# Performance work log

Hardware: AMD Instinct MI355X
Metric: run time of the kernel (lower is better)

The kernel has to match this reference:

```python
import jax, jax.numpy as jnp
import numpy as np

D = 512          # token_dim * num_heads
TOKEN_DIM = 256
SCALE = TOKEN_DIM ** (-0.5)


def _l2norm(x, axis):
    # torch.nn.functional.normalize: x / max(||x||_2, eps)
    n = jnp.linalg.norm(x, axis=axis, keepdims=True)
    return x / jnp.maximum(n, 1e-12)


def setup_inputs() -> dict:
    key = jax.random.key(0)
    ks = jax.random.split(key, 32)
    B, N, IN = 8, 4096, 512
    s_in = 1.0 / np.sqrt(IN)
    s_d = 1.0 / np.sqrt(D)

    def lin(k, fin, fout, scale):
        kw, kb = jax.random.split(k)
        return (jax.random.uniform(kw, (fin, fout), jnp.float32, -scale, scale),
                jax.random.uniform(kb, (fout,), jnp.float32, -scale, scale))

    wq_I, bq_I = lin(ks[0], IN, D, s_in)
    wk_I, bk_I = lin(ks[1], IN, D, s_in)
    wq_M, bq_M = lin(ks[2], IN, D, s_in)
    wk_M, bk_M = lin(ks[3], IN, D, s_in)
    p1_w, p1_b = lin(ks[4], D, D, s_d)
    p2_w, p2_b = lin(ks[5], D, D, s_d)
    p3_w, p3_b = lin(ks[6], D, D, s_d)
    p4_w, p4_b = lin(ks[7], D, D, s_d)
    f_w, f_b = lin(ks[8], D, TOKEN_DIM, s_d)
    return {
        'x_I': jax.random.normal(ks[9], (B, N, IN), jnp.float32),
        'x_M': jax.random.normal(ks[10], (B, N, IN), jnp.float32),
        'wq_I': wq_I, 'bq_I': bq_I, 'wk_I': wk_I, 'bk_I': bk_I,
        'wq_M': wq_M, 'bq_M': bq_M, 'wk_M': wk_M, 'bk_M': bk_M,
        'wg_I': jax.random.normal(ks[11], (D, 1), jnp.float32),
        'wg_M': jax.random.normal(ks[12], (D, 1), jnp.float32),
        'p1_w': p1_w, 'p1_b': p1_b, 'p2_w': p2_w, 'p2_b': p2_b,
        'p3_w': p3_w, 'p3_b': p3_b, 'p4_w': p4_w, 'p4_b': p4_b,
        'f_w': f_w, 'f_b': f_b,
    }


def reference(x_I, x_M, wq_I, bq_I, wk_I, bk_I, wq_M, bq_M, wk_M, bk_M,
              wg_I, wg_M, p1_w, p1_b, p2_w, p2_b, p3_w, p3_b, p4_w, p4_b,
              f_w, f_b):
    # projections, then L2-normalize along feature dim
    q_I = _l2norm(x_I @ wq_I + bq_I, axis=-1)   # [B, N, D]
    k_I = _l2norm(x_I @ wk_I + bk_I, axis=-1)
    q_M = _l2norm(x_M @ wq_M + bq_M, axis=-1)
    k_M = _l2norm(x_M @ wk_M + bk_M, axis=-1)

    # softmax-free attention weights, L2-normalized over sequence dim
    A_I = _l2norm((q_I @ wg_I) * SCALE, axis=1)  # [B, N, 1]
    A_M = _l2norm((q_M @ wg_M) * SCALE, axis=1)

    # pooled global queries, broadcast back over tokens
    G_I = jnp.sum(A_I * q_I, axis=1, keepdims=True)  # [B, 1, D]
    G_M = jnp.sum(A_M * q_M, axis=1, keepdims=True)

    out = ((G_I * k_I) @ p1_w + p1_b
           + (G_I * k_M) @ p2_w + p2_b
           + (G_M * k_M) @ p3_w + p3_b
           + (G_M * k_I) @ p4_w + p4_b
           + q_I + q_M)                              # [B, N, D]
    return out @ f_w + f_b                           # [B, N, token_dim]
```

## Files before the change

kernel.cpp:

```cpp
#include <hip/hip_runtime.h>

typedef unsigned short u16;
typedef unsigned int   u32;
typedef __bf16 bf16_t;
typedef bf16_t bf16x8 __attribute__((ext_vector_type(8)));
typedef float  f32x4  __attribute__((ext_vector_type(4)));

__device__ __forceinline__ float b2f(u16 u){
  u32 x = ((u32)u) << 16;
  return __builtin_bit_cast(float, x);
}
__device__ __forceinline__ u16 f2b(float f){
  u32 u = __builtin_bit_cast(u32, f);
  u32 r = u + 0x7FFFu + ((u >> 16) & 1u);
  return (u16)(r >> 16);
}

union V8 { uint4 q; u16 u[8]; };

__device__ __forceinline__ void gld16(const u16* gsrc, u16* ldst){
  __builtin_amdgcn_global_load_lds(
      (const __attribute__((address_space(1))) u32*)gsrc,
      (__attribute__((address_space(3))) u32*)ldst, 16, 0, 0);
}


struct CArgs { const float* src[4]; u16* dst[4]; int cnt[4]; };

__global__ __launch_bounds__(256) void convert_k(CArgs c){
  int z = blockIdx.z;
  int i8 = (blockIdx.x * 256 + threadIdx.x) * 8;
  if (i8 >= c.cnt[z]) return;
  const float* s = c.src[z] + i8;
  float4 a = *(const float4*)s;
  float4 b = *(const float4*)(s + 4);
  V8 o;
  o.u[0]=f2b(a.x); o.u[1]=f2b(a.y); o.u[2]=f2b(a.z); o.u[3]=f2b(a.w);
  o.u[4]=f2b(b.x); o.u[5]=f2b(b.y); o.u[6]=f2b(b.z); o.u[7]=f2b(b.w);
  *(uint4*)(c.dst[z] + i8) = o.q;
}

struct TArgs { const float* src[5]; u16* dst[5]; int ncol[5]; };

__global__ __launch_bounds__(256) void transpose_k(TArgs t,
    const float* __restrict__ p1b, const float* __restrict__ p2b,
    const float* __restrict__ p3b, const float* __restrict__ p4b,
    const float* __restrict__ fw, const float* __restrict__ fb,
    float* __restrict__ cb, float* __restrict__ Gun)
{
  __shared__ u16 T[64][65];
  __shared__ float sb[512];
  int z = blockIdx.z;
  int tid = threadIdx.x;
  if (z == 5){
    if (blockIdx.x == 0 && blockIdx.y == 0){
      sb[tid]       = p1b[tid] + p2b[tid] + p3b[tid] + p4b[tid];
      sb[tid + 256] = p1b[tid+256] + p2b[tid+256] + p3b[tid+256] + p4b[tid+256];
      __syncthreads();
      float acc = 0.f;
      for (int j = 0; j < 512; j++) acc += sb[j] * fw[j*256 + tid];
      cb[tid] = acc + fb[tid];
    } else if (blockIdx.x >= 1 && blockIdx.x <= 4){
      int idx = ((blockIdx.x - 1)*8 + blockIdx.y)*256 + tid;
      Gun[idx] = 0.f;
    }
    return;
  }
  int nc = t.ncol[z];
  int j0 = blockIdx.y * 64;
  if (j0 >= nc) return;
  int i0 = blockIdx.x * 64;
  const float* s = t.src[z];
  u16* d = t.dst[z];
  #pragma unroll
  for (int rep = 0; rep < 16; rep++){
    int lin = rep*256 + tid;
    int r = lin >> 6, c = lin & 63;
    T[c][r] = f2b(s[(size_t)(i0 + r) * nc + j0 + c]);
  }
  __syncthreads();
  #pragma unroll
  for (int rep = 0; rep < 16; rep++){
    int lin = rep*256 + tid;
    int r = lin >> 6, c = lin & 63;
    d[(size_t)(j0 + r) * 512 + i0 + c] = T[r][c];
  }
}

__global__ __launch_bounds__(256, 2) void proj_k(
    const float* __restrict__ XI, const float* __restrict__ XM,
    const u16* __restrict__ WTI, const u16* __restrict__ WTM,
    const float* __restrict__ bqI, const float* __restrict__ bkI,
    const float* __restrict__ bqM, const float* __restrict__ bkM,
    const float* __restrict__ wgI, const float* __restrict__ wgM,
    u16* __restrict__ qI, u16* __restrict__ kI,
    u16* __restrict__ qM, u16* __restrict__ kM,
    float* __restrict__ Araw, float* __restrict__ Gun)
{
  const int tid = threadIdx.x, l = tid & 63, w = tid >> 6;
  const int m0 = blockIdx.x * 64;
  const int y  = blockIdx.y, zi = blockIdx.z;
  __shared__ __align__(16) u16 As[2][64*32];
  __shared__ __align__(16) u16 Bs[2][4][4096];
  const int lr = l & 15, quad = l >> 4;
  const int srow = l >> 2;
  const int swz8 = ((l & 3) ^ ((l >> 3) & 3)) * 8;
  const int aqs8 = (quad ^ ((lr >> 1) & 3)) * 8;
  const int wn = w * 128;

  const float* X  = zi ? XM : XI;
  const u16* Wbase = (zi ? WTM : WTI) + (size_t)y * 512 * 512 + (size_t)wn * 512;
  const float* bias = y ? (zi ? bkM : bkI) : (zi ? bqM : bqI);
  const float* wg   = zi ? wgM : wgI;
  u16* OUT = y ? (zi ? kM : kI) : (zi ? qM : qI);

  const int arow = w*16 + (l >> 2);
  const int aks  = (l & 3) * 8;
  const float* aptr = X + (size_t)(m0 + arow)*512 + aks;

  f32x4 acc[4][8] = {};
  float4 s0a, s0b, s1a, s1b;

  s0a = *(const float4*)(aptr);
  s0b = *(const float4*)(aptr + 4);
  __builtin_amdgcn_sched_barrier(0);
  #pragma unroll
  for (int i = 0; i < 8; i++)
    gld16(Wbase + (size_t)(i*16 + srow)*512 + swz8, &Bs[0][w][i*512]);
  __builtin_amdgcn_sched_barrier(0);
  s1a = *(const float4*)(aptr + 32);
  s1b = *(const float4*)(aptr + 36);
  __builtin_amdgcn_sched_barrier(0);
  {
    V8 o;
    o.u[0]=f2b(s0a.x); o.u[1]=f2b(s0a.y); o.u[2]=f2b(s0a.z); o.u[3]=f2b(s0a.w);
    o.u[4]=f2b(s0b.x); o.u[5]=f2b(s0b.y); o.u[6]=f2b(s0b.z); o.u[7]=f2b(s0b.w);
    *(uint4*)&As[0][arow*32 + swz8] = o.q;
  }
  asm volatile("s_waitcnt vmcnt(2)" ::: "memory");
  asm volatile("s_waitcnt lgkmcnt(0)" ::: "memory");
  __builtin_amdgcn_sched_barrier(0);
  __builtin_amdgcn_s_barrier();

#define PBODY(P, CV0, CV1, LD0, LD1, KA, KB, DOLOAD, VMC) do{                              \
    bf16x8 aF[4], bF[8];                                                                   \
    _Pragma("unroll")                                                                      \
    for (int mt = 0; mt < 4; mt++)                                                         \
      aF[mt] = *(const bf16x8*)&As[(P)][(mt*16 + lr)*32 + aqs8];                           \
    _Pragma("unroll")                                                                      \
    for (int nt = 0; nt < 8; nt++)                                                         \
      bF[nt] = *(const bf16x8*)&Bs[(P)][w][(nt*16 + lr)*32 + aqs8];                        \
    __builtin_amdgcn_sched_barrier(0);                                                     \
    _Pragma("unroll")                                                                      \
    for (int i = 0; i < 8; i++)                                                            \
      gld16(Wbase + (size_t)(i*16 + srow)*512 + (KB) + swz8, &Bs[(P)^1][w][i*512]);        \
    __builtin_amdgcn_sched_barrier(0);                                                     \
    if (DOLOAD){                                                                           \
      LD0 = *(const float4*)(aptr + (KA));                                                 \
      LD1 = *(const float4*)(aptr + (KA) + 4);                                             \
    }                                                                                      \
    __builtin_amdgcn_sched_barrier(0);                                                     \
    { V8 o;                                                                                \
      o.u[0]=f2b((CV0).x); o.u[1]=f2b((CV0).y); o.u[2]=f2b((CV0).z); o.u[3]=f2b((CV0).w); \
      o.u[4]=f2b((CV1).x); o.u[5]=f2b((CV1).y); o.u[6]=f2b((CV1).z); o.u[7]=f2b((CV1).w); \
      *(uint4*)&As[(P)^1][arow*32 + swz8] = o.q; }                                         \
    __builtin_amdgcn_s_setprio(1);                                                         \
    _Pragma("unroll")                                                                      \
    for (int mt = 0; mt < 4; mt++){                                                        \
      _Pragma("unroll")                                                                    \
      for (int nt = 0; nt < 8; nt++)                                                       \
        acc[mt][nt] = __builtin_amdgcn_mfma_f32_16x16x32_bf16(aF[mt], bF[nt], acc[mt][nt], 0, 0, 0); \
    }                                                                                      \
    __builtin_amdgcn_s_setprio(0);                                                         \
    asm volatile("s_waitcnt vmcnt(" #VMC ")" ::: "memory");                                \
    asm volatile("s_waitcnt lgkmcnt(0)" ::: "memory");                                     \
    __builtin_amdgcn_sched_barrier(0);                                                     \
    __builtin_amdgcn_s_barrier();                                                          \
  } while(0)

  for (int tt = 0; tt < 7; ++tt){
    PBODY(0, s1a, s1b, s0a, s0b, (2*tt+2)*32, (2*tt+1)*32, 1, 2);
    PBODY(1, s0a, s0b, s1a, s1b, (2*tt+3)*32, (2*tt+2)*32, 1, 2);
  }
  PBODY(0, s1a, s1b, s0a, s0b, 0, 480, 0, 0);
  {
    bf16x8 aF[4], bF[8];
    #pragma unroll
    for (int mt = 0; mt < 4; mt++)
      aF[mt] = *(const bf16x8*)&As[1][(mt*16 + lr)*32 + aqs8];
    #pragma unroll
    for (int nt = 0; nt < 8; nt++)
      bF[nt] = *(const bf16x8*)&Bs[1][w][(nt*16 + lr)*32 + aqs8];
    __builtin_amdgcn_s_setprio(1);
    #pragma unroll
    for (int mt = 0; mt < 4; mt++){
      #pragma unroll
      for (int nt = 0; nt < 8; nt++)
        acc[mt][nt] = __builtin_amdgcn_mfma_f32_16x16x32_bf16(aF[mt], bF[nt], acc[mt][nt], 0, 0, 0);
    }
    __builtin_amdgcn_s_setprio(0);
  }
#undef PBODY

  float wgv[8];
  if (y == 0){
    #pragma unroll
    for (int nt = 0; nt < 8; nt++) wgv[nt] = wg[wn + nt*16 + lr];
  }
  #pragma unroll
  for (int nt = 0; nt < 8; nt++){
    float bcol = bias[wn + nt*16 + lr];
    #pragma unroll
    for (int mt = 0; mt < 4; mt++)
      #pragma unroll
      for (int r = 0; r < 4; r++)
        acc[mt][nt][r] += bcol;
  }
  float ss[4][4], dq[4][4];
  #pragma unroll
  for (int mt = 0; mt < 4; mt++)
    #pragma unroll
    for (int r = 0; r < 4; r++){
      float s = 0.f, d = 0.f;
      #pragma unroll
      for (int nt = 0; nt < 8; nt++){
        float v = acc[mt][nt][r];
        s += v*v;
        if (y == 0) d += v * wgv[nt];
      }
      ss[mt][r] = s; dq[mt][r] = d;
    }
  #pragma unroll
  for (int off = 1; off < 16; off <<= 1){
    #pragma unroll
    for (int mt = 0; mt < 4; mt++)
      #pragma unroll
      for (int r = 0; r < 4; r++){
        ss[mt][r] += __shfl_xor(ss[mt][r], off, 64);
        if (y == 0) dq[mt][r] += __shfl_xor(dq[mt][r], off, 64);
      }
  }
  __syncthreads();
  float* red    = (float*)As;
  float* red2   = red + 256;
  float* rnS    = red2 + 256;
  float* araw_s = rnS + 64;
  if (lr == 0){
    #pragma unroll
    for (int mt = 0; mt < 4; mt++)
      #pragma unroll
      for (int r = 0; r < 4; r++){
        int row = mt*16 + quad*4 + r;
        red[w*64 + row] = ss[mt][r];
        if (y == 0) red2[w*64 + row] = dq[mt][r];
      }
  }
  __syncthreads();
  if (tid < 64){
    float t2 = red[tid] + red[64+tid] + red[128+tid] + red[192+tid];
    float rn = 1.f / fmaxf(sqrtf(t2), 1e-12f);
    rnS[tid] = rn;
    if (y == 0){
      float d = red2[tid] + red2[64+tid] + red2[128+tid] + red2[192+tid];
      float a = d * rn * 0.0625f;
      araw_s[tid] = a;
      Araw[zi*32768 + m0 + tid] = a;
    }
  }
  __syncthreads();
  float part[8] = {};
  #pragma unroll
  for (int mt = 0; mt < 4; mt++){
    f32x4 rn4 = *(const f32x4*)&rnS[mt*16 + quad*4];
    #pragma unroll
    for (int r = 0; r < 4; r++){
      float aw = (y == 0) ? araw_s[mt*16 + quad*4 + r] : 0.f;
      #pragma unroll
      for (int nt = 0; nt < 8; nt++){
        float v = acc[mt][nt][r] * rn4[r];
        OUT[(size_t)(m0 + mt*16 + quad*4 + r)*512 + wn + nt*16 + lr] = f2b(v);
        if (y == 0) part[nt] += aw * v;
      }
    }
  }
  if (y == 0){
    #pragma unroll
    for (int nt = 0; nt < 8; nt++){
      part[nt] += __shfl_xor(part[nt], 16, 64);
      part[nt] += __shfl_xor(part[nt], 32, 64);
    }
    if (quad == 0){
      int bb = blockIdx.x >> 6;
      #pragma unroll
      for (int nt = 0; nt < 8; nt++)
        atomicAdd(&Gun[((size_t)zi*8 + bb)*512 + wn + nt*16 + lr], part[nt]);
    }
  }
}

template<int MODE>
__global__ __launch_bounds__(256, 2) void gemm2_k(
    const u16* __restrict__ A0, const u16* __restrict__ A1,
    const u16* __restrict__ A2, const u16* __restrict__ A3,
    const u16* __restrict__ BT,
    const float* __restrict__ cb,
    u16* __restrict__ Cq, float* __restrict__ Cf)
{
  constexpr int KTOT = (MODE == 2) ? 2048 : 512;
  constexpr int NT   = KTOT / 32;
  const int tid = threadIdx.x, l = tid & 63, w = tid >> 6;
  const int m0 = blockIdx.x * 128, n0 = blockIdx.y * 128;
  __shared__ __align__(16) u16 S[4][2][4096];
  f32x4 acc[4][4] = {};
  const int wm = (w >> 1) * 64, wn = (w & 1) * 64;
  const int lr = l & 15, quad = l >> 4;
  const int srow = l >> 2;
  const int swz8 = ((l & 3) ^ ((l >> 3) & 3)) * 8;
  const int aqs8 = (quad ^ ((lr >> 1) & 3)) * 8;

  const u16* Bbase = BT;
  u16* Cqb = Cq;
  if constexpr (MODE == 2)
    Bbase = BT + (size_t)(m0 >> 12) * 256 * 2048;
  if constexpr (MODE == 1){
    Bbase = BT + (size_t)blockIdx.z * 262144;
    Cqb   = Cq + (size_t)blockIdx.z * 131072;
  }

  auto stage = [&](int kk, int buf) __attribute__((always_inline)) {
    const u16* Ab; int kloc;
    if constexpr (MODE == 2){
      int which = kk >> 9; kloc = kk & 511;
      Ab = (which == 0) ? A0 : (which == 1) ? A1 : (which == 2) ? A2 : A3;
    } else { Ab = A0; kloc = kk; }
    #pragma unroll
    for (int i = 0; i < 2; i++){
      int r = w*32 + i*16 + srow;
      gld16(Ab    + (size_t)(m0 + r) * 512  + kloc + swz8, &S[buf][0][(w*2 + i)*512]);
      gld16(Bbase + (size_t)(n0 + r) * KTOT + kk   + swz8, &S[buf][1][(w*2 + i)*512]);
    }
  };

  stage(0, 0);
  stage(32, 1);
  stage(64, 2);
  asm volatile("s_waitcnt vmcnt(8)" ::: "memory");
  __builtin_amdgcn_sched_barrier(0);
  __builtin_amdgcn_s_barrier();

  for (int t = 0; t < NT; ++t){
    const u16* Sc = &S[t & 3][0][0];
    bf16x8 aF[4], bF[4];
    #pragma unroll
    for (int mt = 0; mt < 4; mt++)
      aF[mt] = *(const bf16x8*)&Sc[(wm + mt*16 + lr)*32 + aqs8];
    #pragma unroll
    for (int nt = 0; nt < 4; nt++)
      bF[nt] = *(const bf16x8*)&Sc[4096 + (wn + nt*16 + lr)*32 + aqs8];
    if (t < NT - 1){
      int kn = (t + 3 < NT) ? (t + 3)*32 : 0;
      stage(kn, (t + 3) & 3);
    }
    __builtin_amdgcn_s_setprio(1);
    #pragma unroll
    for (int mt = 0; mt < 4; mt++){
      #pragma unroll
      for (int nt = 0; nt < 4; nt++)
        acc[mt][nt] = __builtin_amdgcn_mfma_f32_16x16x32_bf16(aF[mt], bF[nt], acc[mt][nt], 0, 0, 0);
    }
    __builtin_amdgcn_s_setprio(0);
    if (t < NT - 1){
      asm volatile("s_waitcnt vmcnt(8)" ::: "memory");
      __builtin_amdgcn_sched_barrier(0);
      __builtin_amdgcn_s_barrier();
    }
  }
  asm volatile("s_waitcnt vmcnt(0)" ::: "memory");

  #pragma unroll
  for (int nt = 0; nt < 4; nt++){
    int col = n0 + wn + nt*16 + lr;
    #pragma unroll
    for (int mt = 0; mt < 4; mt++){
      int row0 = m0 + wm + mt*16 + quad*4;
      #pragma unroll
      for (int r = 0; r < 4; r++){
        int row = row0 + r;
        float v = acc[mt][nt][r];
        if constexpr (MODE == 1){
          Cqb[(size_t)row*512 + col] = f2b(v);
        } else {
          Cf[(size_t)row*256 + col] = v + cb[col];
        }
      }
    }
  }
}

__global__ __launch_bounds__(256) void ranorm_k(const float* __restrict__ Araw,
                                                float* __restrict__ rA){
  int idx = blockIdx.x;
  const float* A = Araw + idx*4096;
  int tid = threadIdx.x, l = tid & 63, w = tid >> 6;
  float ss = 0.f;
  for (int i = tid; i < 4096; i += 256){ float a = A[i]; ss += a*a; }
  #pragma unroll
  for (int off = 32; off > 0; off >>= 1) ss += __shfl_xor(ss, off, 64);
  __shared__ float red[4];
  if (l == 0) red[w] = ss;
  __syncthreads();
  if (tid == 0)
    rA[idx] = 1.f / fmaxf(sqrtf(red[0] + red[1] + red[2] + red[3]), 1e-12f);
}

__global__ __launch_bounds__(256) void weff_k(
    const u16* __restrict__ pfT, const u16* __restrict__ fT,
    const float* __restrict__ Gun, const float* __restrict__ rA,
    u16* __restrict__ WT)
{
  int b = blockIdx.x, o = blockIdx.y, tid = threadIdx.x;
  int k0 = tid * 8;
  V8 out;
  if (k0 < 1024){
    int kk = k0 & 511;
    const u16* pa = pfT + ((k0 < 512) ? 0      : 131072) + o*512 + kk;
    const u16* pb = pfT + ((k0 < 512) ? 393216 : 262144) + o*512 + kk;
    float rI = rA[b], rM = rA[8 + b];
    const float* gI = Gun + b*512 + kk;
    const float* gM = Gun + 4096 + b*512 + kk;
    V8 Pa, Pb; Pa.q = *(const uint4*)pa; Pb.q = *(const uint4*)pb;
    float4 gi0 = *(const float4*)gI, gi1 = *(const float4*)(gI+4);
    float4 gm0 = *(const float4*)gM, gm1 = *(const float4*)(gM+4);
    float gi[8] = {gi0.x,gi0.y,gi0.z,gi0.w,gi1.x,gi1.y,gi1.z,gi1.w};
    float gm[8] = {gm0.x,gm0.y,gm0.z,gm0.w,gm1.x,gm1.y,gm1.z,gm1.w};
    #pragma unroll
    for (int j = 0; j < 8; j++)
      out.u[j] = f2b(rI*gi[j]*b2f(Pa.u[j]) + rM*gm[j]*b2f(Pb.u[j]));
  } else {
    out.q = *(const uint4*)(fT + o*512 + (k0 & 511));
  }
  *(uint4*)(WT + ((size_t)b*256 + o)*2048 + k0) = out.q;
}

extern "C" void kernel_launch(void* const* d_in, const int* in_sizes, int n_in,
                              void* d_out, int out_size, void* d_ws, size_t ws_size,
                              hipStream_t stream)
{
  const float* x_I  = (const float*)d_in[0];
  const float* x_M  = (const float*)d_in[1];
  const float* wq_I = (const float*)d_in[2];
  const float* bq_I = (const float*)d_in[3];
  const float* wk_I = (const float*)d_in[4];
  const float* bk_I = (const float*)d_in[5];
  const float* wq_M = (const float*)d_in[6];
  const float* bq_M = (const float*)d_in[7];
  const float* wk_M = (const float*)d_in[8];
  const float* bk_M = (const float*)d_in[9];
  const float* wg_I = (const float*)d_in[10];
  const float* wg_M = (const float*)d_in[11];
  const float* p1_w = (const float*)d_in[12];
  const float* p1_b = (const float*)d_in[13];
  const float* p2_w = (const float*)d_in[14];
  const float* p2_b = (const float*)d_in[15];
  const float* p3_w = (const float*)d_in[16];
  const float* p3_b = (const float*)d_in[17];
  const float* p4_w = (const float*)d_in[18];
  const float* p4_b = (const float*)d_in[19];
  const float* f_w  = (const float*)d_in[20];
  const float* f_b  = (const float*)d_in[21];

  char* ws = (char*)d_ws;
  u16*  wqkT_I = (u16*)(ws + 0);
  u16*  wqkT_M = (u16*)(ws + 1048576);
  u16*  fT     = (u16*)(ws + 2097152);
  u16*  pcat   = (u16*)(ws + 2359296);
  u16*  pfT    = (u16*)(ws + 4456448);
  u16*  WT     = (u16*)(ws + 5505024);
  float* cb    = (float*)(ws + 13893632);
  float* Araw  = (float*)(ws + 13894656);
  float* rA    = (float*)(ws + 14156800);
  float* Gun   = (float*)(ws + 14157056);
  u16*  qIb    = (u16*)(ws + 14189824);
  u16*  kIb    = (u16*)(ws + 47744256);
  u16*  qMb    = (u16*)(ws + 81298688);
  u16*  kMb    = (u16*)(ws + 114853120);

  CArgs c;
  const float* csrc[4] = {p1_w, p2_w, p3_w, p4_w};
  u16* cdst[4] = {pcat, pcat + 262144, pcat + 524288, pcat + 786432};
  for (int i = 0; i < 4; i++){ c.src[i] = csrc[i]; c.dst[i] = cdst[i]; c.cnt[i] = 262144; }
  convert_k<<<dim3(128,1,4), 256, 0, stream>>>(c);

  TArgs t;
  const float* tsrc[5] = {wq_I, wk_I, wq_M, wk_M, f_w};
  u16* tdst[5] = {wqkT_I, wqkT_I + 262144, wqkT_M, wqkT_M + 262144, fT};
  int tnc[5] = {512, 512, 512, 512, 256};
  for (int i = 0; i < 5; i++){ t.src[i] = tsrc[i]; t.dst[i] = tdst[i]; t.ncol[i] = tnc[i]; }
  transpose_k<<<dim3(8,8,6), 256, 0, stream>>>(t, p1_b, p2_b, p3_b, p4_b, f_w, f_b, cb, Gun);

  gemm2_k<1><<<dim3(2,4,4), 256, 0, stream>>>(fT, nullptr, nullptr, nullptr,
      pcat, nullptr, pfT, nullptr);

  proj_k<<<dim3(512,2,2), 256, 0, stream>>>(x_I, x_M, wqkT_I, wqkT_M,
      bq_I, bk_I, bq_M, bk_M, wg_I, wg_M, qIb, kIb, qMb, kMb, Araw, Gun);

  ranorm_k<<<16, 256, 0, stream>>>(Araw, rA);

  weff_k<<<dim3(8,256), 256, 0, stream>>>(pfT, fT, Gun, rA, WT);

  gemm2_k<2><<<dim3(256,2), 256, 0, stream>>>(kIb, kMb, qIb, qMb,
      WT, cb, nullptr, (float*)d_out);
}
```

Before: 384.2 us.

## Load weight operands directly from global into registers, dropping LDS staging

In both the projection kernel and the second GEMM kernel, the weight (B) fragments are now read straight from global memory into registers each k-step instead of being staged through shared memory with async global-to-LDS copies. Only the activation (A) tile still goes through LDS. This halves LDS use per block and lets gemm2 request three resident blocks per CU instead of two, aiming to raise occupancy and cut LDS traffic. The cost is that the B loads sit right before the MFMAs in each iteration. Because vmcnt waits retire loads in issue order, waiting on them can also force the earlier prefetched A loads to finish, which may expose global/L2 latency and collapse the prefetch pipeline depth.

New measurement: 455.3 us. 1.18x slower.

```diff
diff --git a/kernel.cpp b/kernel.cpp
--- a/kernel.cpp
+++ b/kernel.cpp
@@ -101,15 +101,13 @@
   const int m0 = blockIdx.x * 64;
   const int y  = blockIdx.y, zi = blockIdx.z;
   __shared__ __align__(16) u16 As[2][64*32];
-  __shared__ __align__(16) u16 Bs[2][4][4096];
   const int lr = l & 15, quad = l >> 4;
-  const int srow = l >> 2;
   const int swz8 = ((l & 3) ^ ((l >> 3) & 3)) * 8;
   const int aqs8 = (quad ^ ((lr >> 1) & 3)) * 8;
   const int wn = w * 128;
 
   const float* X  = zi ? XM : XI;
-  const u16* Wbase = (zi ? WTM : WTI) + (size_t)y * 512 * 512 + (size_t)wn * 512;
+  const u16* Wb = (zi ? WTM : WTI) + (size_t)y * 512 * 512 + (size_t)wn * 512;
   const float* bias = y ? (zi ? bkM : bkI) : (zi ? bqM : bqI);
   const float* wg   = zi ? wgM : wgI;
   u16* OUT = y ? (zi ? kM : kI) : (zi ? qM : qI);
@@ -123,44 +121,32 @@
 
   s0a = *(const float4*)(aptr);
   s0b = *(const float4*)(aptr + 4);
-  __builtin_amdgcn_sched_barrier(0);
-  #pragma unroll
-  for (int i = 0; i < 8; i++)
-    gld16(Wbase + (size_t)(i*16 + srow)*512 + swz8, &Bs[0][w][i*512]);
-  __builtin_amdgcn_sched_barrier(0);
   s1a = *(const float4*)(aptr + 32);
   s1b = *(const float4*)(aptr + 36);
-  __builtin_amdgcn_sched_barrier(0);
   {
     V8 o;
     o.u[0]=f2b(s0a.x); o.u[1]=f2b(s0a.y); o.u[2]=f2b(s0a.z); o.u[3]=f2b(s0a.w);
     o.u[4]=f2b(s0b.x); o.u[5]=f2b(s0b.y); o.u[6]=f2b(s0b.z); o.u[7]=f2b(s0b.w);
     *(uint4*)&As[0][arow*32 + swz8] = o.q;
   }
-  asm volatile("s_waitcnt vmcnt(2)" ::: "memory");
   asm volatile("s_waitcnt lgkmcnt(0)" ::: "memory");
   __builtin_amdgcn_sched_barrier(0);
   __builtin_amdgcn_s_barrier();
 
-#define PBODY(P, CV0, CV1, LD0, LD1, KA, KB, DOLOAD, VMC) do{                              \
-    bf16x8 aF[4], bF[8];                                                                   \
+#define PBODY(P, CV0, CV1, LD0, LD1, KA, KT, DOLOAD, DOBAR) do{                            \
+    bf16x8 bF[8];                                                                          \
+    _Pragma("unroll")                                                                      \
+    for (int nt = 0; nt < 8; nt++)                                                         \
+      bF[nt] = *(const bf16x8*)&Wb[(size_t)(nt*16 + lr)*512 + (KT) + quad*8];              \
+    bf16x8 aF[4];                                                                          \
     _Pragma("unroll")                                                                      \
     for (int mt = 0; mt < 4; mt++)                                                         \
       aF[mt] = *(const bf16x8*)&As[(P)][(mt*16 + lr)*32 + aqs8];                           \
-    _Pragma("unroll")                                                                      \
-    for (int nt = 0; nt < 8; nt++)                                                         \
-      bF[nt] = *(const bf16x8*)&Bs[(P)][w][(nt*16 + lr)*32 + aqs8];                        \
-    __builtin_amdgcn_sched_barrier(0);                                                     \
-    _Pragma("unroll")                                                                      \
-    for (int i = 0; i < 8; i++)                                                            \
-      gld16(Wbase + (size_t)(i*16 + srow)*512 + (KB) + swz8, &Bs[(P)^1][w][i*512]);        \
-    __builtin_amdgcn_sched_barrier(0);                                                     \
     if (DOLOAD){                                                                           \
       LD0 = *(const float4*)(aptr + (KA));                                                 \
       LD1 = *(const float4*)(aptr + (KA) + 4);                                             \
     }                                                                                      \
-    __builtin_amdgcn_sched_barrier(0);                                                     \
-    { V8 o;                                                                                \
+    if (DOBAR){ V8 o;                                                                      \
       o.u[0]=f2b((CV0).x); o.u[1]=f2b((CV0).y); o.u[2]=f2b((CV0).z); o.u[3]=f2b((CV0).w); \
       o.u[4]=f2b((CV1).x); o.u[5]=f2b((CV1).y); o.u[6]=f2b((CV1).z); o.u[7]=f2b((CV1).w); \
       *(uint4*)&As[(P)^1][arow*32 + swz8] = o.q; }                                         \
@@ -172,34 +158,19 @@
         acc[mt][nt] = __builtin_amdgcn_mfma_f32_16x16x32_bf16(aF[mt], bF[nt], acc[mt][nt], 0, 0, 0); \
     }                                                                                      \
     __builtin_amdgcn_s_setprio(0);                                                         \
-    asm volatile("s_waitcnt vmcnt(" #VMC ")" ::: "memory");                                \
-    asm volatile("s_waitcnt lgkmcnt(0)" ::: "memory");                                     \
-    __builtin_amdgcn_sched_barrier(0);                                                     \
-    __builtin_amdgcn_s_barrier();                                                          \
+    if (DOBAR){                                                                            \
+      asm volatile("s_waitcnt lgkmcnt(0)" ::: "memory");                                   \
+      __builtin_amdgcn_sched_barrier(0);                                                   \
+      __builtin_amdgcn_s_barrier();                                                        \
+    }                                                                                      \
   } while(0)
 
   for (int tt = 0; tt < 7; ++tt){
-    PBODY(0, s1a, s1b, s0a, s0b, (2*tt+2)*32, (2*tt+1)*32, 1, 2);
-    PBODY(1, s0a, s0b, s1a, s1b, (2*tt+3)*32, (2*tt+2)*32, 1, 2);
-  }
-  PBODY(0, s1a, s1b, s0a, s0b, 0, 480, 0, 0);
-  {
-    bf16x8 aF[4], bF[8];
-    #pragma unroll
-    for (int mt = 0; mt < 4; mt++)
-      aF[mt] = *(const bf16x8*)&As[1][(mt*16 + lr)*32 + aqs8];
-    #pragma unroll
-    for (int nt = 0; nt < 8; nt++)
-      bF[nt] = *(const bf16x8*)&Bs[1][w][(nt*16 + lr)*32 + aqs8];
-    __builtin_amdgcn_s_setprio(1);
-    #pragma unroll
-    for (int mt = 0; mt < 4; mt++){
-      #pragma unroll
-      for (int nt = 0; nt < 8; nt++)
-        acc[mt][nt] = __builtin_amdgcn_mfma_f32_16x16x32_bf16(aF[mt], bF[nt], acc[mt][nt], 0, 0, 0);
-    }
-    __builtin_amdgcn_s_setprio(0);
-  }
+    PBODY(0, s1a, s1b, s0a, s0b, (2*tt+2)*32, (2*tt)*32,   1, 1);
+    PBODY(1, s0a, s0b, s1a, s1b, (2*tt+3)*32, (2*tt+1)*32, 1, 1);
+  }
+  PBODY(0, s1a, s1b, s0a, s0b, 0, 448, 0, 1);
+  PBODY(1, s0a, s0b, s1a, s1b, 0, 480, 0, 0);
 #undef PBODY
 
   float wgv[8];
@@ -299,7 +270,7 @@
 }
 
 template<int MODE>
-__global__ __launch_bounds__(256, 2) void gemm2_k(
+__global__ __launch_bounds__(256, 3) void gemm2_k(
     const u16* __restrict__ A0, const u16* __restrict__ A1,
     const u16* __restrict__ A2, const u16* __restrict__ A3,
     const u16* __restrict__ BT,
@@ -310,7 +281,7 @@
   constexpr int NT   = KTOT / 32;
   const int tid = threadIdx.x, l = tid & 63, w = tid >> 6;
   const int m0 = blockIdx.x * 128, n0 = blockIdx.y * 128;
-  __shared__ __align__(16) u16 S[4][2][4096];
+  __shared__ __align__(16) u16 SA[4][4096];
   f32x4 acc[4][4] = {};
   const int wm = (w >> 1) * 64, wn = (w & 1) * 64;
   const int lr = l & 15, quad = l >> 4;
@@ -326,8 +297,9 @@
     Bbase = BT + (size_t)blockIdx.z * 262144;
     Cqb   = Cq + (size_t)blockIdx.z * 131072;
   }
-
-  auto stage = [&](int kk, int buf) __attribute__((always_inline)) {
+  const u16* Bb = Bbase + (size_t)(n0 + wn) * KTOT;
+
+  auto stageA = [&](int kk, int buf) __attribute__((always_inline)) {
     const u16* Ab; int kloc;
     if constexpr (MODE == 2){
       int which = kk >> 9; kloc = kk & 511;
@@ -336,30 +308,29 @@
     #pragma unroll
     for (int i = 0; i < 2; i++){
       int r = w*32 + i*16 + srow;
-      gld16(Ab    + (size_t)(m0 + r) * 512  + kloc + swz8, &S[buf][0][(w*2 + i)*512]);
-      gld16(Bbase + (size_t)(n0 + r) * KTOT + kk   + swz8, &S[buf][1][(w*2 + i)*512]);
+      gld16(Ab + (size_t)(m0 + r) * 512 + kloc + swz8, &SA[buf][(w*2 + i)*512]);
     }
   };
 
-  stage(0, 0);
-  stage(32, 1);
-  stage(64, 2);
-  asm volatile("s_waitcnt vmcnt(8)" ::: "memory");
+  stageA(0, 0);
+  stageA(32, 1);
+  stageA(64, 2);
+  asm volatile("s_waitcnt vmcnt(4)" ::: "memory");
   __builtin_amdgcn_sched_barrier(0);
   __builtin_amdgcn_s_barrier();
 
   for (int t = 0; t < NT; ++t){
-    const u16* Sc = &S[t & 3][0][0];
-    bf16x8 aF[4], bF[4];
+    bf16x8 bF[4];
+    #pragma unroll
+    for (int nt = 0; nt < 4; nt++)
+      bF[nt] = *(const bf16x8*)&Bb[(size_t)(nt*16 + lr)*KTOT + t*32 + quad*8];
+    bf16x8 aF[4];
     #pragma unroll
     for (int mt = 0; mt < 4; mt++)
-      aF[mt] = *(const bf16x8*)&Sc[(wm + mt*16 + lr)*32 + aqs8];
-    #pragma unroll
-    for (int nt = 0; nt < 4; nt++)
-      bF[nt] = *(const bf16x8*)&Sc[4096 + (wn + nt*16 + lr)*32 + aqs8];
+      aF[mt] = *(const bf16x8*)&SA[t & 3][(wm + mt*16 + lr)*32 + aqs8];
     if (t < NT - 1){
       int kn = (t + 3 < NT) ? (t + 3)*32 : 0;
-      stage(kn, (t + 3) & 3);
+      stageA(kn, (t + 3) & 3);
     }
     __builtin_amdgcn_s_setprio(1);
     #pragma unroll
@@ -370,7 +341,8 @@
     }
     __builtin_amdgcn_s_setprio(0);
     if (t < NT - 1){
-      asm volatile("s_waitcnt vmcnt(8)" ::: "memory");
+      __builtin_amdgcn_sched_barrier(0);
+      asm volatile("s_waitcnt vmcnt(4)" ::: "memory");
       __builtin_amdgcn_sched_barrier(0);
       __builtin_amdgcn_s_barrier();
     }
```

## Fold weight conversion into transpose launch; cut GEMM ring to three stages for occupancy

Applied to the files above, without the earlier changes.

The separate fp32-to-bf16 conversion kernel for the p1..p4 weights is merged into the transpose kernel as extra z-slices, saving one launch. The output GEMM's LDS ring shrinks from four to three stages (prefetch depth two) so launch bounds can request three blocks per CU. The final GEMM also remaps block indices so consecutive blocks span different M regions. The trade-off is higher occupancy against a shallower prefetch, which exposes more load latency per block.

After: 374.1 us. 1.03x faster.

```diff
diff --git a/kernel.cpp b/kernel.cpp
--- a/kernel.cpp
+++ b/kernel.cpp
@@ -25,24 +25,11 @@
 }
 
 
-struct CArgs { const float* src[4]; u16* dst[4]; int cnt[4]; };
-
-__global__ __launch_bounds__(256) void convert_k(CArgs c){
-  int z = blockIdx.z;
-  int i8 = (blockIdx.x * 256 + threadIdx.x) * 8;
-  if (i8 >= c.cnt[z]) return;
-  const float* s = c.src[z] + i8;
-  float4 a = *(const float4*)s;
-  float4 b = *(const float4*)(s + 4);
-  V8 o;
-  o.u[0]=f2b(a.x); o.u[1]=f2b(a.y); o.u[2]=f2b(a.z); o.u[3]=f2b(a.w);
-  o.u[4]=f2b(b.x); o.u[5]=f2b(b.y); o.u[6]=f2b(b.z); o.u[7]=f2b(b.w);
-  *(uint4*)(c.dst[z] + i8) = o.q;
-}
+struct CArgs { const float* src[4]; u16* dst[4]; };
 
 struct TArgs { const float* src[5]; u16* dst[5]; int ncol[5]; };
 
-__global__ __launch_bounds__(256) void transpose_k(TArgs t,
+__global__ __launch_bounds__(256) void transpose_k(TArgs t, CArgs c,
     const float* __restrict__ p1b, const float* __restrict__ p2b,
     const float* __restrict__ p3b, const float* __restrict__ p4b,
     const float* __restrict__ fw, const float* __restrict__ fb,
@@ -52,6 +39,22 @@
   __shared__ float sb[512];
   int z = blockIdx.z;
   int tid = threadIdx.x;
+  if (z >= 6){
+    int zz = z - 6;
+    int i16 = ((blockIdx.x*8 + blockIdx.y)*256 + tid) * 16;
+    const float* s = c.src[zz] + i16;
+    u16* d = c.dst[zz] + i16;
+    #pragma unroll
+    for (int h = 0; h < 2; h++){
+      float4 a = *(const float4*)(s + h*8);
+      float4 b = *(const float4*)(s + h*8 + 4);
+      V8 o;
+      o.u[0]=f2b(a.x); o.u[1]=f2b(a.y); o.u[2]=f2b(a.z); o.u[3]=f2b(a.w);
+      o.u[4]=f2b(b.x); o.u[5]=f2b(b.y); o.u[6]=f2b(b.z); o.u[7]=f2b(b.w);
+      *(uint4*)(d + h*8) = o.q;
+    }
+    return;
+  }
   if (z == 5){
     if (blockIdx.x == 0 && blockIdx.y == 0){
       sb[tid]       = p1b[tid] + p2b[tid] + p3b[tid] + p4b[tid];
@@ -75,15 +78,15 @@
   #pragma unroll
   for (int rep = 0; rep < 16; rep++){
     int lin = rep*256 + tid;
-    int r = lin >> 6, c = lin & 63;
-    T[c][r] = f2b(s[(size_t)(i0 + r) * nc + j0 + c]);
+    int r = lin >> 6, cc = lin & 63;
+    T[cc][r] = f2b(s[(size_t)(i0 + r) * nc + j0 + cc]);
   }
   __syncthreads();
   #pragma unroll
   for (int rep = 0; rep < 16; rep++){
     int lin = rep*256 + tid;
-    int r = lin >> 6, c = lin & 63;
-    d[(size_t)(j0 + r) * 512 + i0 + c] = T[r][c];
+    int r = lin >> 6, cc = lin & 63;
+    d[(size_t)(j0 + r) * 512 + i0 + cc] = T[r][cc];
   }
 }
 
@@ -299,7 +302,7 @@
 }
 
 template<int MODE>
-__global__ __launch_bounds__(256, 2) void gemm2_k(
+__global__ __launch_bounds__(256, 3) void gemm2_k(
     const u16* __restrict__ A0, const u16* __restrict__ A1,
     const u16* __restrict__ A2, const u16* __restrict__ A3,
     const u16* __restrict__ BT,
@@ -309,8 +312,11 @@
   constexpr int KTOT = (MODE == 2) ? 2048 : 512;
   constexpr int NT   = KTOT / 32;
   const int tid = threadIdx.x, l = tid & 63, w = tid >> 6;
-  const int m0 = blockIdx.x * 128, n0 = blockIdx.y * 128;
-  __shared__ __align__(16) u16 S[4][2][4096];
+  int bx = blockIdx.x;
+  if constexpr (MODE == 2)
+    bx = ((blockIdx.x & 7) << 5) | (blockIdx.x >> 3);
+  const int m0 = bx * 128, n0 = blockIdx.y * 128;
+  __shared__ __align__(16) u16 S[3][2][4096];
   f32x4 acc[4][4] = {};
   const int wm = (w >> 1) * 64, wn = (w & 1) * 64;
   const int lr = l & 15, quad = l >> 4;
@@ -343,13 +349,13 @@
 
   stage(0, 0);
   stage(32, 1);
-  stage(64, 2);
-  asm volatile("s_waitcnt vmcnt(8)" ::: "memory");
+  asm volatile("s_waitcnt vmcnt(4)" ::: "memory");
   __builtin_amdgcn_sched_barrier(0);
   __builtin_amdgcn_s_barrier();
 
+  int bc = 0;
   for (int t = 0; t < NT; ++t){
-    const u16* Sc = &S[t & 3][0][0];
+    const u16* Sc = &S[bc][0][0];
     bf16x8 aF[4], bF[4];
     #pragma unroll
     for (int mt = 0; mt < 4; mt++)
@@ -358,8 +364,9 @@
     for (int nt = 0; nt < 4; nt++)
       bF[nt] = *(const bf16x8*)&Sc[4096 + (wn + nt*16 + lr)*32 + aqs8];
     if (t < NT - 1){
-      int kn = (t + 3 < NT) ? (t + 3)*32 : 0;
-      stage(kn, (t + 3) & 3);
+      int kn = (t + 2 < NT) ? (t + 2)*32 : 0;
+      int bs = bc + 2; if (bs >= 3) bs -= 3;
+      stage(kn, bs);
     }
     __builtin_amdgcn_s_setprio(1);
     #pragma unroll
@@ -370,10 +377,12 @@
     }
     __builtin_amdgcn_s_setprio(0);
     if (t < NT - 1){
-      asm volatile("s_waitcnt vmcnt(8)" ::: "memory");
+      __builtin_amdgcn_sched_barrier(0);
+      asm volatile("s_waitcnt vmcnt(4)" ::: "memory");
       __builtin_amdgcn_sched_barrier(0);
       __builtin_amdgcn_s_barrier();
     }
+    bc = (bc == 2) ? 0 : bc + 1;
   }
   asm volatile("s_waitcnt vmcnt(0)" ::: "memory");
 
@@ -485,18 +494,17 @@
   u16*  qMb    = (u16*)(ws + 81298688);
   u16*  kMb    = (u16*)(ws + 114853120);
 
+  TArgs t;
   CArgs c;
-  const float* csrc[4] = {p1_w, p2_w, p3_w, p4_w};
-  u16* cdst[4] = {pcat, pcat + 262144, pcat + 524288, pcat + 786432};
-  for (int i = 0; i < 4; i++){ c.src[i] = csrc[i]; c.dst[i] = cdst[i]; c.cnt[i] = 262144; }
-  convert_k<<<dim3(128,1,4), 256, 0, stream>>>(c);
-
-  TArgs t;
   const float* tsrc[5] = {wq_I, wk_I, wq_M, wk_M, f_w};
   u16* tdst[5] = {wqkT_I, wqkT_I + 262144, wqkT_M, wqkT_M + 262144, fT};
   int tnc[5] = {512, 512, 512, 512, 256};
   for (int i = 0; i < 5; i++){ t.src[i] = tsrc[i]; t.dst[i] = tdst[i]; t.ncol[i] = tnc[i]; }
-  transpose_k<<<dim3(8,8,6), 256, 0, stream>>>(t, p1_b, p2_b, p3_b, p4_b, f_w, f_b, cb, Gun);
+  const float* csrc[4] = {p1_w, p2_w, p3_w, p4_w};
+  u16* cdst[4] = {pcat, pcat + 262144, pcat + 524288, pcat + 786432};
+  for (int i = 0; i < 4; i++){ c.src[i] = csrc[i]; c.dst[i] = cdst[i]; }
+  transpose_k<<<dim3(8,8,10), 256, 0, stream>>>(t, c, p1_b, p2_b, p3_b, p4_b,
+                                                f_w, f_b, cb, Gun);
 
   gemm2_k<1><<<dim3(2,4,4), 256, 0, stream>>>(fT, nullptr, nullptr, nullptr,
       pcat, nullptr, pfT, nullptr);
```
